# Performance work log

Hardware: AMD Instinct MI355X
Metric: run time of the kernel (lower is better)

## Reference

```python
import jax, jax.numpy as jnp
import numpy as np
from jax import lax


def setup_inputs() -> dict:
    key = jax.random.key(0)
    ks = jax.random.split(key, 13)
    B, L, H, E, V, T = 32, 256, 512, 512, 32000, 64
    s = 0.05
    return {
        "z": jax.random.normal(ks[0], (B, L), jnp.float32),
        "embedding": jax.random.normal(ks[1], (V, E), jnp.float32) * s,
        "Wh": jax.random.normal(ks[2], (H, L), jnp.float32) * s,
        "bh": jax.random.normal(ks[3], (H,), jnp.float32) * s,
        "Wc": jax.random.normal(ks[4], (H, L), jnp.float32) * s,
        "bc": jax.random.normal(ks[5], (H,), jnp.float32) * s,
        "Wih": jax.random.normal(ks[6], (4 * H, E), jnp.float32) * s,
        "Whh": jax.random.normal(ks[7], (4 * H, H), jnp.float32) * s,
        "bih": jax.random.normal(ks[8], (4 * H,), jnp.float32) * s,
        "bhh": jax.random.normal(ks[9], (4 * H,), jnp.float32) * s,
        "Wfc": jax.random.normal(ks[10], (V, H), jnp.float32) * s,
        "bfc": jax.random.normal(ks[11], (V,), jnp.float32) * s,
        "context_length": T,
    }


def reference(z, embedding, Wh, bh, Wc, bc, Wih, Whh, bih, bhh, Wfc, bfc, context_length):
    # project latent to initial LSTM state: [B, H]
    h0 = z @ Wh.T + bh
    c0 = z @ Wc.T + bc
    b_gates = bih + bhh

    def step(carry, _):
        h, c, x = carry  # each [B, H] / [B, E]
        gates = x @ Wih.T + h @ Whh.T + b_gates  # [B, 4H] (pytorch gate order i,f,g,o)
        i, f, g, o = jnp.split(gates, 4, axis=-1)
        c_new = jax.nn.sigmoid(f) * c + jax.nn.sigmoid(i) * jnp.tanh(g)
        h_new = jax.nn.sigmoid(o) * jnp.tanh(c_new)
        logits = h_new @ Wfc.T + bfc  # [B, V]
        pred = jnp.argmax(logits, axis=-1)  # greedy token
        x_new = embedding[pred]  # [B, E]
        return (h_new, c_new, x_new), logits

    # first step feeds h itself as the input (x is None in torch code)
    _, logits = lax.scan(step, (h0, c0, h0), None, length=context_length)
    return jnp.transpose(logits, (1, 0, 2))  # [B, T, V]
```

## Files before the change

### kernel.cpp

```cpp
#include <hip/hip_runtime.h>
#include <hip/hip_bf16.h>
#include <cstdint>
#include <cstddef>

#define NB 32
#define NL 256
#define NH 512
#define NE 512
#define NV 32000
#define NT 64
#define NJ 2048
#define NK 1024
#define NKT 16

typedef __attribute__((ext_vector_type(8))) short bf16x8;
typedef __attribute__((ext_vector_type(4))) float f32x4;


__device__ __forceinline__ unsigned int sortable_f32(float f) {
  unsigned int s = __float_as_uint(f);
  return (s & 0x80000000u) ? ~s : (s | 0x80000000u);
}

__device__ __forceinline__ unsigned long long pack_key(float f, int v) {
  return ((unsigned long long)sortable_f32(f) << 32) |
         (unsigned long long)(unsigned int)(~v);
}

__device__ __forceinline__ unsigned long long shfl_xor_u64(unsigned long long x, int m) {
  unsigned int lo = (unsigned int)x;
  unsigned int hi = (unsigned int)(x >> 32);
  lo = __shfl_xor(lo, m, 64);
  hi = __shfl_xor(hi, m, 64);
  return ((unsigned long long)hi << 32) | lo;
}

__device__ __forceinline__ uint32_t pack_hi16(uint32_t u0, uint32_t u1) {
  return __builtin_amdgcn_perm(u1, u0, 0x07060302u);
}

__device__ __forceinline__ void split3(float4 wa, float4 wb,
                                       bf16x8& A1, bf16x8& A2, bf16x8& A3) {
  union U { uint32_t w[4]; bf16x8 v; };
  U u1, u2, u3;
  float e[8] = {wa.x, wa.y, wa.z, wa.w, wb.x, wb.y, wb.z, wb.w};
#pragma unroll
  for (int p = 0; p < 4; ++p) {
    float e0 = e[2 * p], e1 = e[2 * p + 1];
    uint32_t a0 = __float_as_uint(e0), a1 = __float_as_uint(e1);
    u1.w[p] = pack_hi16(a0, a1);
    float r0 = e0 - __uint_as_float(a0 & 0xffff0000u);
    float r1 = e1 - __uint_as_float(a1 & 0xffff0000u);
    uint32_t b0 = __float_as_uint(r0), b1 = __float_as_uint(r1);
    u2.w[p] = pack_hi16(b0, b1);
    float q0 = r0 - __uint_as_float(b0 & 0xffff0000u);
    float q1 = r1 - __uint_as_float(b1 & 0xffff0000u);
    u3.w[p] = pack_hi16(__float_as_uint(q0), __float_as_uint(q1));
  }
  A1 = u1.v; A2 = u2.v; A3 = u3.v;
}


__global__ void k_init(const float* __restrict__ z, const float* __restrict__ Wh,
                       const float* __restrict__ bh, const float* __restrict__ Wc,
                       const float* __restrict__ bc, float* __restrict__ hbuf,
                       float* __restrict__ cbuf, unsigned long long* __restrict__ keys) {
  int idx = blockIdx.x * 256 + threadIdx.x;
  int b = idx >> 9, hh = idx & 511;
  const float* zr  = z + b * NL;
  const float* whr = Wh + hh * NL;
  const float* wcr = Wc + hh * NL;
  float ah = 0.f, ac = 0.f;
  for (int k = 0; k < NL; ++k) {
    float zv = zr[k];
    ah += zv * whr[k];
    ac += zv * wcr[k];
  }
  hbuf[b * NH + hh] = ah + bh[hh];
  cbuf[b * NH + hh] = ac + bc[hh];
  if (idx < 64) keys[idx] = 0ULL;
}

__global__ void k_transposeW(const float* __restrict__ Wih, const float* __restrict__ Whh,
                             float* __restrict__ WT) {
  __shared__ float tile[32][33];
  int j0 = blockIdx.x * 32;
  int k0 = blockIdx.y * 32;
  int tx = threadIdx.x & 31;
  int ty = threadIdx.x >> 5;
  for (int r = ty; r < 32; r += 8) {
    int j = j0 + r, k = k0 + tx;
    tile[r][tx] = (k < NE) ? Wih[j * NE + k] : Whh[j * NH + (k - NE)];
  }
  __syncthreads();
  for (int r = ty; r < 32; r += 8) {
    int k = k0 + r, j = j0 + tx;
    WT[(size_t)k * NJ + j] = tile[tx][r];
  }
}

__global__ void k_gates(const float* __restrict__ WT, const float* __restrict__ emb,
                        const float* __restrict__ hbuf, const unsigned long long* __restrict__ keys,
                        float* __restrict__ partials, int step) {
  int tid  = threadIdx.x;
  int jthr = tid & 63, bthr = tid >> 6;
  int j0 = blockIdx.x * 256 + jthr * 4;
  int k0 = blockIdx.y * 64;
  int b0 = bthr * 8;
  const float* hin = hbuf + (size_t)(step & 1) * NB * NH;

  const float* xp[8];
  bool isx = (k0 < NE);
#pragma unroll
  for (int i = 0; i < 8; ++i) {
    int b = b0 + i;
    if (!isx) {
      xp[i] = hin + (size_t)b * NH - NE;
    } else if (step == 0) {
      xp[i] = hin + (size_t)b * NE;
    } else {
      unsigned long long key = keys[((step - 1) & 1) * NB + b];
      unsigned int pred = ~(unsigned int)(key & 0xFFFFFFFFu);
      xp[i] = emb + (size_t)pred * NE;
    }
  }

  float acc[4][8];
#pragma unroll
  for (int jj = 0; jj < 4; ++jj)
#pragma unroll
    for (int i = 0; i < 8; ++i) acc[jj][i] = 0.f;

#pragma unroll 4
  for (int k = k0; k < k0 + 64; ++k) {
    float4 w = *(const float4*)(WT + (size_t)k * NJ + j0);
#pragma unroll
    for (int i = 0; i < 8; ++i) {
      float xv = xp[i][k];
      acc[0][i] += w.x * xv;
      acc[1][i] += w.y * xv;
      acc[2][i] += w.z * xv;
      acc[3][i] += w.w * xv;
    }
  }

  int kt = blockIdx.y;
#pragma unroll
  for (int jj = 0; jj < 4; ++jj)
#pragma unroll
    for (int i = 0; i < 8; ++i)
      partials[((size_t)(j0 + jj) * NB + (b0 + i)) * NKT + kt] = acc[jj][i];
}

__global__ void k_cell(const float* __restrict__ partials, const float* __restrict__ bih,
                       const float* __restrict__ bhh, float* __restrict__ hbuf,
                       float* __restrict__ cbuf, unsigned short* __restrict__ hs,
                       unsigned long long* __restrict__ keys, int step) {
  int idx = blockIdx.x * 256 + threadIdx.x;
  int b = idx >> 9, hh = idx & 511;
  float g4[4];
#pragma unroll
  for (int g = 0; g < 4; ++g) {
    int j = g * NH + hh;
    const float4* p4 = (const float4*)(partials + ((size_t)j * NB + b) * NKT);
    float4 a0 = p4[0], a1 = p4[1], a2 = p4[2], a3 = p4[3];
    float s = ((a0.x + a0.y) + (a0.z + a0.w)) + ((a1.x + a1.y) + (a1.z + a1.w)) +
              ((a2.x + a2.y) + (a2.z + a2.w)) + ((a3.x + a3.y) + (a3.z + a3.w));
    g4[g] = s + bih[j] + bhh[j];
  }
  float ig = 1.0f / (1.0f + expf(-g4[0]));
  float fg = 1.0f / (1.0f + expf(-g4[1]));
  float gg = tanhf(g4[2]);
  float og = 1.0f / (1.0f + expf(-g4[3]));
  float c  = cbuf[b * NH + hh];
  float cn = fg * c + ig * gg;
  float hn = og * tanhf(cn);
  cbuf[b * NH + hh] = cn;
  hbuf[(size_t)((step + 1) & 1) * NB * NH + b * NH + hh] = hn;

  uint32_t u = __float_as_uint(hn);
  float r1 = hn - __uint_as_float(u & 0xffff0000u);
  uint32_t u2 = __float_as_uint(r1);
  float r2 = r1 - __uint_as_float(u2 & 0xffff0000u);
  uint32_t u3 = __float_as_uint(r2);
  hs[0 * NB * NH + b * NH + hh] = (unsigned short)(u >> 16);
  hs[1 * NB * NH + b * NH + hh] = (unsigned short)(u2 >> 16);
  hs[2 * NB * NH + b * NH + hh] = (unsigned short)(u3 >> 16);

  if (idx < NB) keys[(step & 1) * NB + idx] = 0ULL;
}

__global__ __launch_bounds__(256) void k_logits_mfma(
    const float* __restrict__ Wfc, const float* __restrict__ bfc,
    const unsigned short* __restrict__ hs, float* __restrict__ out,
    unsigned long long* __restrict__ keys, int step) {
  __shared__ union {
    unsigned short h[3][32][264];
    float t[32][68];
  } lds;
  __shared__ unsigned long long kmax[32];

  int tid = threadIdx.x;
  int lane = tid & 63, wid = tid >> 6;
  int g = lane >> 4, r16 = lane & 15;
  int vwave = blockIdx.x * 64 + wid * 16;

  if (tid < 32) kmax[tid] = 0ULL;

  f32x4 acc0 = {0.f, 0.f, 0.f, 0.f};
  f32x4 acc1 = {0.f, 0.f, 0.f, 0.f};

  const float* wrow = Wfc + (size_t)(vwave + r16) * NH + g * 8;

  for (int half = 0; half < 2; ++half) {
    __syncthreads();
#pragma unroll
    for (int i = 0; i < 12; ++i) {
      int idx = tid + i * 256;
      int s = idx >> 10, rem = idx & 1023;
      int row = rem >> 5, ch = rem & 31;
      float4 d = *(const float4*)(hs + (size_t)s * (NB * NH) + row * NH + half * 256 + ch * 8);
      *(float4*)(&lds.h[s][row][ch * 8]) = d;
    }
    __syncthreads();

#pragma unroll 2
    for (int kq = 0; kq < 8; ++kq) {
      int k0 = half * 256 + kq * 32;
      float4 wa = *(const float4*)(wrow + k0);
      float4 wb = *(const float4*)(wrow + k0 + 4);
      bf16x8 A1, A2, A3;
      split3(wa, wb, A1, A2, A3);

      int koff = kq * 32 + g * 8;
      bf16x8 B1n0 = *(const bf16x8*)(&lds.h[0][r16][koff]);
      bf16x8 B1n1 = *(const bf16x8*)(&lds.h[0][r16 + 16][koff]);
      bf16x8 B2n0 = *(const bf16x8*)(&lds.h[1][r16][koff]);
      bf16x8 B2n1 = *(const bf16x8*)(&lds.h[1][r16 + 16][koff]);
      bf16x8 B3n0 = *(const bf16x8*)(&lds.h[2][r16][koff]);
      bf16x8 B3n1 = *(const bf16x8*)(&lds.h[2][r16 + 16][koff]);

      acc0 = __builtin_amdgcn_mfma_f32_16x16x32_bf16(A1, B1n0, acc0, 0, 0, 0);
      acc0 = __builtin_amdgcn_mfma_f32_16x16x32_bf16(A1, B2n0, acc0, 0, 0, 0);
      acc0 = __builtin_amdgcn_mfma_f32_16x16x32_bf16(A2, B1n0, acc0, 0, 0, 0);
      acc0 = __builtin_amdgcn_mfma_f32_16x16x32_bf16(A2, B2n0, acc0, 0, 0, 0);
      acc0 = __builtin_amdgcn_mfma_f32_16x16x32_bf16(A1, B3n0, acc0, 0, 0, 0);
      acc0 = __builtin_amdgcn_mfma_f32_16x16x32_bf16(A3, B1n0, acc0, 0, 0, 0);

      acc1 = __builtin_amdgcn_mfma_f32_16x16x32_bf16(A1, B1n1, acc1, 0, 0, 0);
      acc1 = __builtin_amdgcn_mfma_f32_16x16x32_bf16(A1, B2n1, acc1, 0, 0, 0);
      acc1 = __builtin_amdgcn_mfma_f32_16x16x32_bf16(A2, B1n1, acc1, 0, 0, 0);
      acc1 = __builtin_amdgcn_mfma_f32_16x16x32_bf16(A2, B2n1, acc1, 0, 0, 0);
      acc1 = __builtin_amdgcn_mfma_f32_16x16x32_bf16(A1, B3n1, acc1, 0, 0, 0);
      acc1 = __builtin_amdgcn_mfma_f32_16x16x32_bf16(A3, B1n1, acc1, 0, 0, 0);
    }
  }

  float4 bv = *(const float4*)(bfc + vwave + g * 4);
  float lg0[4], lg1[4];
  unsigned long long key0 = 0ULL, key1 = 0ULL;
#pragma unroll
  for (int reg = 0; reg < 4; ++reg) {
    int v = vwave + 4 * g + reg;
    float bvr = (reg == 0) ? bv.x : (reg == 1) ? bv.y : (reg == 2) ? bv.z : bv.w;
    lg0[reg] = acc0[reg] + bvr;
    lg1[reg] = acc1[reg] + bvr;
    unsigned long long p0 = pack_key(lg0[reg], v);
    unsigned long long p1 = pack_key(lg1[reg], v);
    key0 = (p0 > key0) ? p0 : key0;
    key1 = (p1 > key1) ? p1 : key1;
  }
#pragma unroll
  for (int m = 16; m <= 32; m <<= 1) {
    unsigned long long o0 = shfl_xor_u64(key0, m);
    unsigned long long o1 = shfl_xor_u64(key1, m);
    key0 = (o0 > key0) ? o0 : key0;
    key1 = (o1 > key1) ? o1 : key1;
  }
  if (g == 0) {
    atomicMax(&kmax[r16], key0);
    atomicMax(&kmax[r16 + 16], key1);
  }
  __syncthreads();

#pragma unroll
  for (int reg = 0; reg < 4; ++reg) {
    int vloc = wid * 16 + 4 * g + reg;
    lds.t[r16][vloc] = lg0[reg];
    lds.t[r16 + 16][vloc] = lg1[reg];
  }
  __syncthreads();

  {
    int b = tid >> 3, seg = tid & 7;
    float4 p0 = *(const float4*)(&lds.t[b][seg * 8]);
    float4 p1 = *(const float4*)(&lds.t[b][seg * 8 + 4]);
    float* dst = out + ((size_t)b * NT + step) * NV + blockIdx.x * 64 + seg * 8;
    *(float4*)(dst) = p0;
    *(float4*)(dst + 4) = p1;
  }
  if (tid < 32) atomicMax(&keys[(step & 1) * NB + tid], kmax[tid]);
}


extern "C" void kernel_launch(void* const* d_in, const int* in_sizes, int n_in,
                              void* d_out, int out_size, void* d_ws, size_t ws_size,
                              hipStream_t stream) {
  (void)in_sizes; (void)n_in; (void)out_size; (void)ws_size;
  const float* z   = (const float*)d_in[0];
  const float* emb = (const float*)d_in[1];
  const float* Wh  = (const float*)d_in[2];
  const float* bh  = (const float*)d_in[3];
  const float* Wc  = (const float*)d_in[4];
  const float* bc  = (const float*)d_in[5];
  const float* Wih = (const float*)d_in[6];
  const float* Whh = (const float*)d_in[7];
  const float* bih = (const float*)d_in[8];
  const float* bhh = (const float*)d_in[9];
  const float* Wfc = (const float*)d_in[10];
  const float* bfc = (const float*)d_in[11];
  float* out = (float*)d_out;

  float* ws = (float*)d_ws;
  float* WT       = ws;
  float* partials = ws + 2097152;
  float* hbuf     = ws + 3145728;
  float* cbuf     = ws + 3178496;
  unsigned long long* keys = (unsigned long long*)(ws + 3194880);
  unsigned short* hs = (unsigned short*)(ws + 3195008);

  k_init<<<64, 256, 0, stream>>>(z, Wh, bh, Wc, bc, hbuf, cbuf, keys);
  k_transposeW<<<dim3(64, 32), 256, 0, stream>>>(Wih, Whh, WT);

  for (int t = 0; t < NT; ++t) {
    k_gates<<<dim3(8, 16), 256, 0, stream>>>(WT, emb, hbuf, keys, partials, t);
    k_cell<<<64, 256, 0, stream>>>(partials, bih, bhh, hbuf, cbuf, hs, keys, t);
    k_logits_mfma<<<500, 256, 0, stream>>>(Wfc, bfc, hs, out, keys, t);
  }
}
```

Measured before the change: 3.408 ms.

## Pre-split Wfc into three bf16 planes once and prefetch A fragments in logits kernel

New measurement: 3.782 ms. 11.0% more time.

```diff
diff --git a/kernel.cpp b/kernel.cpp
--- a/kernel.cpp
+++ b/kernel.cpp
@@ -99,6 +99,18 @@
   }
 }
 
+__global__ void k_splitWfc(const float* __restrict__ Wfc, unsigned short* __restrict__ Wsp) {
+  const size_t PS = (size_t)NV * NH;
+  size_t i8 = ((size_t)blockIdx.x * 256 + threadIdx.x) * 8;
+  float4 wa = *(const float4*)(Wfc + i8);
+  float4 wb = *(const float4*)(Wfc + i8 + 4);
+  bf16x8 A1, A2, A3;
+  split3(wa, wb, A1, A2, A3);
+  *(bf16x8*)(Wsp + i8) = A1;
+  *(bf16x8*)(Wsp + PS + i8) = A2;
+  *(bf16x8*)(Wsp + 2 * PS + i8) = A3;
+}
+
 __global__ void k_gates(const float* __restrict__ WT, const float* __restrict__ emb,
                         const float* __restrict__ hbuf, const unsigned long long* __restrict__ keys,
                         float* __restrict__ partials, int step) {
@@ -190,8 +202,8 @@
   if (idx < NB) keys[(step & 1) * NB + idx] = 0ULL;
 }
 
-__global__ __launch_bounds__(256) void k_logits_mfma(
-    const float* __restrict__ Wfc, const float* __restrict__ bfc,
+__global__ __launch_bounds__(256, 2) void k_logits_mfma(
+    const unsigned short* __restrict__ Wsp, const float* __restrict__ bfc,
     const unsigned short* __restrict__ hs, float* __restrict__ out,
     unsigned long long* __restrict__ keys, int step) {
   __shared__ union {
@@ -210,7 +222,8 @@
   f32x4 acc0 = {0.f, 0.f, 0.f, 0.f};
   f32x4 acc1 = {0.f, 0.f, 0.f, 0.f};
 
-  const float* wrow = Wfc + (size_t)(vwave + r16) * NH + g * 8;
+  const size_t PS = (size_t)NV * NH;
+  const unsigned short* wrow = Wsp + (size_t)(vwave + r16) * NH + g * 8;
 
   for (int half = 0; half < 2; ++half) {
     __syncthreads();
@@ -224,14 +237,17 @@
     }
     __syncthreads();
 
-#pragma unroll 2
+    bf16x8 A[8][3];
+#pragma unroll
     for (int kq = 0; kq < 8; ++kq) {
       int k0 = half * 256 + kq * 32;
-      float4 wa = *(const float4*)(wrow + k0);
-      float4 wb = *(const float4*)(wrow + k0 + 4);
-      bf16x8 A1, A2, A3;
-      split3(wa, wb, A1, A2, A3);
-
+      A[kq][0] = *(const bf16x8*)(wrow + k0);
+      A[kq][1] = *(const bf16x8*)(wrow + PS + k0);
+      A[kq][2] = *(const bf16x8*)(wrow + 2 * PS + k0);
+    }
+
+#pragma unroll
+    for (int kq = 0; kq < 8; ++kq) {
       int koff = kq * 32 + g * 8;
       bf16x8 B1n0 = *(const bf16x8*)(&lds.h[0][r16][koff]);
       bf16x8 B1n1 = *(const bf16x8*)(&lds.h[0][r16 + 16][koff]);
@@ -240,19 +256,19 @@
       bf16x8 B3n0 = *(const bf16x8*)(&lds.h[2][r16][koff]);
       bf16x8 B3n1 = *(const bf16x8*)(&lds.h[2][r16 + 16][koff]);
 
-      acc0 = __builtin_amdgcn_mfma_f32_16x16x32_bf16(A1, B1n0, acc0, 0, 0, 0);
-      acc0 = __builtin_amdgcn_mfma_f32_16x16x32_bf16(A1, B2n0, acc0, 0, 0, 0);
-      acc0 = __builtin_amdgcn_mfma_f32_16x16x32_bf16(A2, B1n0, acc0, 0, 0, 0);
-      acc0 = __builtin_amdgcn_mfma_f32_16x16x32_bf16(A2, B2n0, acc0, 0, 0, 0);
-      acc0 = __builtin_amdgcn_mfma_f32_16x16x32_bf16(A1, B3n0, acc0, 0, 0, 0);
-      acc0 = __builtin_amdgcn_mfma_f32_16x16x32_bf16(A3, B1n0, acc0, 0, 0, 0);
-
-      acc1 = __builtin_amdgcn_mfma_f32_16x16x32_bf16(A1, B1n1, acc1, 0, 0, 0);
-      acc1 = __builtin_amdgcn_mfma_f32_16x16x32_bf16(A1, B2n1, acc1, 0, 0, 0);
-      acc1 = __builtin_amdgcn_mfma_f32_16x16x32_bf16(A2, B1n1, acc1, 0, 0, 0);
-      acc1 = __builtin_amdgcn_mfma_f32_16x16x32_bf16(A2, B2n1, acc1, 0, 0, 0);
-      acc1 = __builtin_amdgcn_mfma_f32_16x16x32_bf16(A1, B3n1, acc1, 0, 0, 0);
-      acc1 = __builtin_amdgcn_mfma_f32_16x16x32_bf16(A3, B1n1, acc1, 0, 0, 0);
+      acc0 = __builtin_amdgcn_mfma_f32_16x16x32_bf16(A[kq][0], B1n0, acc0, 0, 0, 0);
+      acc0 = __builtin_amdgcn_mfma_f32_16x16x32_bf16(A[kq][0], B2n0, acc0, 0, 0, 0);
+      acc0 = __builtin_amdgcn_mfma_f32_16x16x32_bf16(A[kq][1], B1n0, acc0, 0, 0, 0);
+      acc0 = __builtin_amdgcn_mfma_f32_16x16x32_bf16(A[kq][1], B2n0, acc0, 0, 0, 0);
+      acc0 = __builtin_amdgcn_mfma_f32_16x16x32_bf16(A[kq][0], B3n0, acc0, 0, 0, 0);
+      acc0 = __builtin_amdgcn_mfma_f32_16x16x32_bf16(A[kq][2], B1n0, acc0, 0, 0, 0);
+
+      acc1 = __builtin_amdgcn_mfma_f32_16x16x32_bf16(A[kq][0], B1n1, acc1, 0, 0, 0);
+      acc1 = __builtin_amdgcn_mfma_f32_16x16x32_bf16(A[kq][0], B2n1, acc1, 0, 0, 0);
+      acc1 = __builtin_amdgcn_mfma_f32_16x16x32_bf16(A[kq][1], B1n1, acc1, 0, 0, 0);
+      acc1 = __builtin_amdgcn_mfma_f32_16x16x32_bf16(A[kq][1], B2n1, acc1, 0, 0, 0);
+      acc1 = __builtin_amdgcn_mfma_f32_16x16x32_bf16(A[kq][0], B3n1, acc1, 0, 0, 0);
+      acc1 = __builtin_amdgcn_mfma_f32_16x16x32_bf16(A[kq][2], B1n1, acc1, 0, 0, 0);
     }
   }
 
@@ -293,11 +309,11 @@
 
   {
     int b = tid >> 3, seg = tid & 7;
-    float4 p0 = *(const float4*)(&lds.t[b][seg * 8]);
-    float4 p1 = *(const float4*)(&lds.t[b][seg * 8 + 4]);
+    f32x4 p0 = *(const f32x4*)(&lds.t[b][seg * 8]);
+    f32x4 p1 = *(const f32x4*)(&lds.t[b][seg * 8 + 4]);
     float* dst = out + ((size_t)b * NT + step) * NV + blockIdx.x * 64 + seg * 8;
-    *(float4*)(dst) = p0;
-    *(float4*)(dst + 4) = p1;
+    __builtin_nontemporal_store(p0, (f32x4*)dst);
+    __builtin_nontemporal_store(p1, (f32x4*)(dst + 4));
   }
   if (tid < 32) atomicMax(&keys[(step & 1) * NB + tid], kmax[tid]);
 }
@@ -328,13 +344,15 @@
   float* cbuf     = ws + 3178496;
   unsigned long long* keys = (unsigned long long*)(ws + 3194880);
   unsigned short* hs = (unsigned short*)(ws + 3195008);
+  unsigned short* Wsp = (unsigned short*)(ws + 3219584);
 
   k_init<<<64, 256, 0, stream>>>(z, Wh, bh, Wc, bc, hbuf, cbuf, keys);
   k_transposeW<<<dim3(64, 32), 256, 0, stream>>>(Wih, Whh, WT);
+  k_splitWfc<<<8000, 256, 0, stream>>>(Wfc, Wsp);
 
   for (int t = 0; t < NT; ++t) {
     k_gates<<<dim3(8, 16), 256, 0, stream>>>(WT, emb, hbuf, keys, partials, t);
     k_cell<<<64, 256, 0, stream>>>(partials, bih, bhh, hbuf, cbuf, hs, keys, t);
-    k_logits_mfma<<<500, 256, 0, stream>>>(Wfc, bfc, hs, out, keys, t);
-  }
-}
+    k_logits_mfma<<<500, 256, 0, stream>>>(Wsp, bfc, hs, out, keys, t);
+  }
+}
```

## Prepack Wfc into bf16 triple-split MFMA layout and widen logits blocks

Applied to the files above, without the earlier changes.

Result: slower. 4.053 ms (+18.9%).

```diff
diff --git a/kernel.cpp b/kernel.cpp
--- a/kernel.cpp
+++ b/kernel.cpp
@@ -58,6 +58,10 @@
     u3.w[p] = pack_hi16(__float_as_uint(q0), __float_as_uint(q1));
   }
   A1 = u1.v; A2 = u2.v; A3 = u3.v;
+}
+
+__device__ __forceinline__ unsigned long long load_key(const unsigned long long* p) {
+  return __hip_atomic_load(p, __ATOMIC_ACQUIRE, __HIP_MEMORY_SCOPE_AGENT);
 }
 
 
@@ -78,7 +82,8 @@
   }
   hbuf[b * NH + hh] = ah + bh[hh];
   cbuf[b * NH + hh] = ac + bc[hh];
-  if (idx < 64) keys[idx] = 0ULL;
+  if (idx < 64)
+    __hip_atomic_store(&keys[idx], 0ULL, __ATOMIC_RELEASE, __HIP_MEMORY_SCOPE_AGENT);
 }
 
 __global__ void k_transposeW(const float* __restrict__ Wih, const float* __restrict__ Whh,
@@ -99,6 +104,26 @@
   }
 }
 
+__global__ void k_packWfc(const float* __restrict__ Wfc, unsigned short* __restrict__ Wpk) {
+  int bid = blockIdx.x;
+  int tid = threadIdx.x;
+  int lane = tid & 63, wv = tid >> 6;
+  int r16 = lane & 15, g = lane >> 4;
+  const float* wr = Wfc + (size_t)(bid * 16 + r16) * NH + g * 8;
+#pragma unroll
+  for (int q = 0; q < 4; ++q) {
+    int kq = wv * 4 + q;
+    float4 wa = *(const float4*)(wr + kq * 32);
+    float4 wb = *(const float4*)(wr + kq * 32 + 4);
+    bf16x8 A1, A2, A3;
+    split3(wa, wb, A1, A2, A3);
+    size_t base = ((size_t)(bid * 16 + kq) * 3) << 9;
+    *(bf16x8*)(Wpk + base + lane * 8) = A1;
+    *(bf16x8*)(Wpk + base + 512 + lane * 8) = A2;
+    *(bf16x8*)(Wpk + base + 1024 + lane * 8) = A3;
+  }
+}
+
 __global__ void k_gates(const float* __restrict__ WT, const float* __restrict__ emb,
                         const float* __restrict__ hbuf, const unsigned long long* __restrict__ keys,
                         float* __restrict__ partials, int step) {
@@ -119,8 +144,9 @@
     } else if (step == 0) {
       xp[i] = hin + (size_t)b * NE;
     } else {
-      unsigned long long key = keys[((step - 1) & 1) * NB + b];
+      unsigned long long key = load_key(&keys[((step - 1) & 1) * NB + b]);
       unsigned int pred = ~(unsigned int)(key & 0xFFFFFFFFu);
+      if (pred >= NV) pred = 0;
       xp[i] = emb + (size_t)pred * NE;
     }
   }
@@ -187,75 +213,69 @@
   hs[1 * NB * NH + b * NH + hh] = (unsigned short)(u2 >> 16);
   hs[2 * NB * NH + b * NH + hh] = (unsigned short)(u3 >> 16);
 
-  if (idx < NB) keys[(step & 1) * NB + idx] = 0ULL;
-}
-
-__global__ __launch_bounds__(256) void k_logits_mfma(
-    const float* __restrict__ Wfc, const float* __restrict__ bfc,
+  if (idx < NB)
+    __hip_atomic_store(&keys[(step & 1) * NB + idx], 0ULL,
+                       __ATOMIC_RELEASE, __HIP_MEMORY_SCOPE_AGENT);
+}
+
+__global__ __launch_bounds__(512, 1) void k_logits3(
+    const unsigned short* __restrict__ Wpk, const float* __restrict__ bfc,
     const unsigned short* __restrict__ hs, float* __restrict__ out,
     unsigned long long* __restrict__ keys, int step) {
-  __shared__ union {
-    unsigned short h[3][32][264];
-    float t[32][68];
-  } lds;
+  __shared__ __align__(16) unsigned short H[3][32][520];
+  __shared__ __align__(16) float tbuf[32][132];
   __shared__ unsigned long long kmax[32];
 
-  int tid = threadIdx.x;
-  int lane = tid & 63, wid = tid >> 6;
-  int g = lane >> 4, r16 = lane & 15;
-  int vwave = blockIdx.x * 64 + wid * 16;
-
+  const int tid = threadIdx.x, bid = blockIdx.x;
+  const int lane = tid & 63, wid = tid >> 6;
+  const int r16 = lane & 15, g = lane >> 4;
+
+#pragma unroll
+  for (int i = 0; i < 12; ++i) {
+    int idx = tid + i * 512;
+    int s = idx >> 11, rem = idx & 2047;
+    int row = rem >> 6, ch = rem & 63;
+    float4 d = *(const float4*)(hs + (size_t)s * (NB * NH) + row * NH + ch * 8);
+    *(float4*)(&H[s][row][ch * 8]) = d;
+  }
   if (tid < 32) kmax[tid] = 0ULL;
+  __syncthreads();
+
+  const int wg = bid * 8 + wid;
+  const unsigned short* wbase = Wpk + (((size_t)wg * 48) << 9) + lane * 8;
 
   f32x4 acc0 = {0.f, 0.f, 0.f, 0.f};
   f32x4 acc1 = {0.f, 0.f, 0.f, 0.f};
 
-  const float* wrow = Wfc + (size_t)(vwave + r16) * NH + g * 8;
-
-  for (int half = 0; half < 2; ++half) {
-    __syncthreads();
-#pragma unroll
-    for (int i = 0; i < 12; ++i) {
-      int idx = tid + i * 256;
-      int s = idx >> 10, rem = idx & 1023;
-      int row = rem >> 5, ch = rem & 31;
-      float4 d = *(const float4*)(hs + (size_t)s * (NB * NH) + row * NH + half * 256 + ch * 8);
-      *(float4*)(&lds.h[s][row][ch * 8]) = d;
-    }
-    __syncthreads();
-
-#pragma unroll 2
-    for (int kq = 0; kq < 8; ++kq) {
-      int k0 = half * 256 + kq * 32;
-      float4 wa = *(const float4*)(wrow + k0);
-      float4 wb = *(const float4*)(wrow + k0 + 4);
-      bf16x8 A1, A2, A3;
-      split3(wa, wb, A1, A2, A3);
-
-      int koff = kq * 32 + g * 8;
-      bf16x8 B1n0 = *(const bf16x8*)(&lds.h[0][r16][koff]);
-      bf16x8 B1n1 = *(const bf16x8*)(&lds.h[0][r16 + 16][koff]);
-      bf16x8 B2n0 = *(const bf16x8*)(&lds.h[1][r16][koff]);
-      bf16x8 B2n1 = *(const bf16x8*)(&lds.h[1][r16 + 16][koff]);
-      bf16x8 B3n0 = *(const bf16x8*)(&lds.h[2][r16][koff]);
-      bf16x8 B3n1 = *(const bf16x8*)(&lds.h[2][r16 + 16][koff]);
-
-      acc0 = __builtin_amdgcn_mfma_f32_16x16x32_bf16(A1, B1n0, acc0, 0, 0, 0);
-      acc0 = __builtin_amdgcn_mfma_f32_16x16x32_bf16(A1, B2n0, acc0, 0, 0, 0);
-      acc0 = __builtin_amdgcn_mfma_f32_16x16x32_bf16(A2, B1n0, acc0, 0, 0, 0);
-      acc0 = __builtin_amdgcn_mfma_f32_16x16x32_bf16(A2, B2n0, acc0, 0, 0, 0);
-      acc0 = __builtin_amdgcn_mfma_f32_16x16x32_bf16(A1, B3n0, acc0, 0, 0, 0);
-      acc0 = __builtin_amdgcn_mfma_f32_16x16x32_bf16(A3, B1n0, acc0, 0, 0, 0);
-
-      acc1 = __builtin_amdgcn_mfma_f32_16x16x32_bf16(A1, B1n1, acc1, 0, 0, 0);
-      acc1 = __builtin_amdgcn_mfma_f32_16x16x32_bf16(A1, B2n1, acc1, 0, 0, 0);
-      acc1 = __builtin_amdgcn_mfma_f32_16x16x32_bf16(A2, B1n1, acc1, 0, 0, 0);
-      acc1 = __builtin_amdgcn_mfma_f32_16x16x32_bf16(A2, B2n1, acc1, 0, 0, 0);
-      acc1 = __builtin_amdgcn_mfma_f32_16x16x32_bf16(A1, B3n1, acc1, 0, 0, 0);
-      acc1 = __builtin_amdgcn_mfma_f32_16x16x32_bf16(A3, B1n1, acc1, 0, 0, 0);
-    }
-  }
-
+#pragma unroll
+  for (int kq = 0; kq < 16; ++kq) {
+    bf16x8 A1 = *(const bf16x8*)(wbase + ((kq * 3 + 0) << 9));
+    bf16x8 A2 = *(const bf16x8*)(wbase + ((kq * 3 + 1) << 9));
+    bf16x8 A3 = *(const bf16x8*)(wbase + ((kq * 3 + 2) << 9));
+    const int ko = kq * 32 + g * 8;
+    bf16x8 B1n0 = *(const bf16x8*)(&H[0][r16][ko]);
+    bf16x8 B1n1 = *(const bf16x8*)(&H[0][r16 + 16][ko]);
+    bf16x8 B2n0 = *(const bf16x8*)(&H[1][r16][ko]);
+    bf16x8 B2n1 = *(const bf16x8*)(&H[1][r16 + 16][ko]);
+    bf16x8 B3n0 = *(const bf16x8*)(&H[2][r16][ko]);
+    bf16x8 B3n1 = *(const bf16x8*)(&H[2][r16 + 16][ko]);
+
+    acc0 = __builtin_amdgcn_mfma_f32_16x16x32_bf16(A1, B1n0, acc0, 0, 0, 0);
+    acc0 = __builtin_amdgcn_mfma_f32_16x16x32_bf16(A1, B2n0, acc0, 0, 0, 0);
+    acc0 = __builtin_amdgcn_mfma_f32_16x16x32_bf16(A2, B1n0, acc0, 0, 0, 0);
+    acc0 = __builtin_amdgcn_mfma_f32_16x16x32_bf16(A2, B2n0, acc0, 0, 0, 0);
+    acc0 = __builtin_amdgcn_mfma_f32_16x16x32_bf16(A1, B3n0, acc0, 0, 0, 0);
+    acc0 = __builtin_amdgcn_mfma_f32_16x16x32_bf16(A3, B1n0, acc0, 0, 0, 0);
+
+    acc1 = __builtin_amdgcn_mfma_f32_16x16x32_bf16(A1, B1n1, acc1, 0, 0, 0);
+    acc1 = __builtin_amdgcn_mfma_f32_16x16x32_bf16(A1, B2n1, acc1, 0, 0, 0);
+    acc1 = __builtin_amdgcn_mfma_f32_16x16x32_bf16(A2, B1n1, acc1, 0, 0, 0);
+    acc1 = __builtin_amdgcn_mfma_f32_16x16x32_bf16(A2, B2n1, acc1, 0, 0, 0);
+    acc1 = __builtin_amdgcn_mfma_f32_16x16x32_bf16(A1, B3n1, acc1, 0, 0, 0);
+    acc1 = __builtin_amdgcn_mfma_f32_16x16x32_bf16(A3, B1n1, acc1, 0, 0, 0);
+  }
+
+  const int vwave = bid * 128 + wid * 16;
   float4 bv = *(const float4*)(bfc + vwave + g * 4);
   float lg0[4], lg1[4];
   unsigned long long key0 = 0ULL, key1 = 0ULL;
@@ -286,18 +306,18 @@
 #pragma unroll
   for (int reg = 0; reg < 4; ++reg) {
     int vloc = wid * 16 + 4 * g + reg;
-    lds.t[r16][vloc] = lg0[reg];
-    lds.t[r16 + 16][vloc] = lg1[reg];
+    tbuf[r16][vloc] = lg0[reg];
+    tbuf[r16 + 16][vloc] = lg1[reg];
   }
   __syncthreads();
 
   {
-    int b = tid >> 3, seg = tid & 7;
-    float4 p0 = *(const float4*)(&lds.t[b][seg * 8]);
-    float4 p1 = *(const float4*)(&lds.t[b][seg * 8 + 4]);
-    float* dst = out + ((size_t)b * NT + step) * NV + blockIdx.x * 64 + seg * 8;
-    *(float4*)(dst) = p0;
-    *(float4*)(dst + 4) = p1;
+    int bb = tid >> 4, seg = tid & 15;
+    f32x4 p0 = *(const f32x4*)(&tbuf[bb][seg * 8]);
+    f32x4 p1 = *(const f32x4*)(&tbuf[bb][seg * 8 + 4]);
+    float* dst = out + ((size_t)bb * NT + step) * NV + bid * 128 + seg * 8;
+    __builtin_nontemporal_store(p0, (f32x4*)dst);
+    __builtin_nontemporal_store(p1, (f32x4*)(dst + 4));
   }
   if (tid < 32) atomicMax(&keys[(step & 1) * NB + tid], kmax[tid]);
 }
@@ -328,13 +348,15 @@
   float* cbuf     = ws + 3178496;
   unsigned long long* keys = (unsigned long long*)(ws + 3194880);
   unsigned short* hs = (unsigned short*)(ws + 3195008);
+  unsigned short* Wpk = (unsigned short*)(ws + 3219584);
 
   k_init<<<64, 256, 0, stream>>>(z, Wh, bh, Wc, bc, hbuf, cbuf, keys);
   k_transposeW<<<dim3(64, 32), 256, 0, stream>>>(Wih, Whh, WT);
+  k_packWfc<<<2000, 256, 0, stream>>>(Wfc, Wpk);
 
   for (int t = 0; t < NT; ++t) {
     k_gates<<<dim3(8, 16), 256, 0, stream>>>(WT, emb, hbuf, keys, partials, t);
     k_cell<<<64, 256, 0, stream>>>(partials, bih, bhh, hbuf, cbuf, hs, keys, t);
-    k_logits_mfma<<<500, 256, 0, stream>>>(Wfc, bfc, hs, out, keys, t);
-  }
-}
+    k_logits3<<<250, 512, 0, stream>>>(Wpk, bfc, hs, out, keys, t);
+  }
+}
```
